# Kernel tuning notes

Measured on AMD Instinct MI355X. Metric: run time of the kernel, lower is better.

Reference implementation:

```python
import jax, jax.numpy as jnp
import numpy as np

EPS = 1e-10
FAR_DELTA = 1e10  # delta appended for the last sample, as in the torch code


def setup_inputs() -> dict:
    key = jax.random.key(0)
    k1, k2, k3 = jax.random.split(key, 3)
    N, P, C = 131072, 128, 3
    density = jax.random.normal(k1, (N, P), dtype=jnp.float32)  # raw density (relu'd inside)
    feature = jax.random.uniform(k2, (N, P, C), dtype=jnp.float32)
    # depth values must be increasing along the sample dim (they come from a ray sampler);
    # build them as a cumulative sum of positive steps in roughly [0, 6].
    steps = jax.random.uniform(k3, (N, P), dtype=jnp.float32) * 0.05
    depth_values = jnp.cumsum(steps, axis=-1) + 1.0
    return {"density": density, "feature": feature, "depth_values": depth_values}


def reference(density, feature, depth_values):
    # deltas: consecutive depth differences, huge delta for the final sample  [N, P]
    deltas = jnp.concatenate(
        [depth_values[:, 1:] - depth_values[:, :-1],
         jnp.full_like(depth_values[:, :1], FAR_DELTA)], axis=-1)
    # alpha = 1 - exp(-relu(density) * delta)   [N, P]
    alpha = 1.0 - jnp.exp(-jax.nn.relu(density) * deltas)
    # transmittance: exclusive cumprod of (1 - alpha + eps)   [N, P]
    trans = jnp.cumprod(
        jnp.concatenate([jnp.ones_like(alpha[:, :1]), 1.0 - alpha + EPS], axis=-1),
        axis=-1)[:, :-1]
    weights = alpha * trans  # [N, P]
    feat_out = jnp.sum(weights[..., None] * feature, axis=1)  # [N, C]
    depth_out = jnp.sum(weights * depth_values, axis=1)       # [N]
    return feat_out, depth_out
```

## Files before the change

### kernel.cpp

```cpp
#include <hip/hip_runtime.h>

#define EPS 1e-10f
#define FAR_DELTA 1e10f

__global__ __launch_bounds__(256) void volrend_kernel(
    const float* __restrict__ density,
    const float* __restrict__ feature,
    const float* __restrict__ depth,
    float* __restrict__ feat_out,
    float* __restrict__ depth_out,
    int N)
{
    const int lane = threadIdx.x & 63;
    const int wave = threadIdx.x >> 6;
    const int ray  = blockIdx.x * 4 + wave;
    if (ray >= N) return;

    const int P = 128;
    const float* dptr = density + (size_t)ray * P;
    const float* zptr = depth   + (size_t)ray * P;
    const float* fptr = feature + (size_t)ray * P * 3;

    float den0 = dptr[lane];
    float den1 = dptr[lane + 64];
    float z0   = zptr[lane];
    float z1   = zptr[lane + 64];

    float zn0 = __shfl_down(z0, 1, 64);
    float z64 = __shfl(z1, 0, 64);
    if (lane == 63) zn0 = z64;
    float zn1 = __shfl_down(z1, 1, 64);

    float delta0 = zn0 - z0;
    float delta1 = (lane == 63) ? FAR_DELTA : (zn1 - z1);

    float t0 = expf(-fmaxf(den0, 0.0f) * delta0);
    float t1 = expf(-fmaxf(den1, 0.0f) * delta1);
    float alpha0 = 1.0f - t0;
    float alpha1 = 1.0f - t1;
    t0 += EPS;
    t1 += EPS;

    float p0 = t0;
    #pragma unroll
    for (int off = 1; off < 64; off <<= 1) {
        float v = __shfl_up(p0, off, 64);
        if (lane >= off) p0 *= v;
    }
    float T0 = __shfl(p0, 63, 64);

    float trans0 = __shfl_up(p0, 1, 64);
    if (lane == 0) trans0 = 1.0f;

    float p1 = t1;
    #pragma unroll
    for (int off = 1; off < 64; off <<= 1) {
        float v = __shfl_up(p1, off, 64);
        if (lane >= off) p1 *= v;
    }
    float trans1 = __shfl_up(p1, 1, 64);
    if (lane == 0) trans1 = 1.0f;
    trans1 *= T0;

    float w0 = alpha0 * trans0;
    float w1 = alpha1 * trans1;

    float f00 = fptr[lane * 3 + 0];
    float f01 = fptr[lane * 3 + 1];
    float f02 = fptr[lane * 3 + 2];
    float f10 = fptr[(lane + 64) * 3 + 0];
    float f11 = fptr[(lane + 64) * 3 + 1];
    float f12 = fptr[(lane + 64) * 3 + 2];

    float acc0 = w0 * f00 + w1 * f10;
    float acc1 = w0 * f01 + w1 * f11;
    float acc2 = w0 * f02 + w1 * f12;
    float accd = w0 * z0  + w1 * z1;

    #pragma unroll
    for (int off = 32; off >= 1; off >>= 1) {
        acc0 += __shfl_xor(acc0, off, 64);
        acc1 += __shfl_xor(acc1, off, 64);
        acc2 += __shfl_xor(acc2, off, 64);
        accd += __shfl_xor(accd, off, 64);
    }

    if (lane == 0) {
        feat_out[ray * 3 + 0] = acc0;
        feat_out[ray * 3 + 1] = acc1;
        feat_out[ray * 3 + 2] = acc2;
        depth_out[ray]        = accd;
    }
}

extern "C" void kernel_launch(void* const* d_in, const int* in_sizes, int n_in,
                              void* d_out, int out_size, void* d_ws, size_t ws_size,
                              hipStream_t stream) {
    const float* density = (const float*)d_in[0];
    const float* feature = (const float*)d_in[1];
    const float* depth   = (const float*)d_in[2];

    const int P = 128;
    const int N = in_sizes[0] / P;

    float* feat_out  = (float*)d_out;
    float* depth_out = (float*)d_out + (size_t)N * 3;

    const int raysPerBlock = 4;
    dim3 grid((N + raysPerBlock - 1) / raysPerBlock);
    dim3 block(256);
    volrend_kernel<<<grid, block, 0, stream>>>(density, feature, depth,
                                               feat_out, depth_out, N);
}
```

Baseline: 349.3 us.

## Process each ray with 16 lanes of 8 samples using float4 loads

Reassigns work so each 16-lane group handles one ray and each thread processes 8 contiguous samples. Density, depth and feature are read with float4 vector loads instead of strided scalar loads. The transmittance scan becomes a per-thread serial product followed by a 16-lane shuffle scan, and the reduction also uses 16 lanes. It also uses fast __expf, which slightly lowers precision.

```diff
diff --git a/kernel.cpp b/kernel.cpp
--- a/kernel.cpp
+++ b/kernel.cpp
@@ -11,85 +11,79 @@
     float* __restrict__ depth_out,
     int N)
 {
-    const int lane = threadIdx.x & 63;
-    const int wave = threadIdx.x >> 6;
-    const int ray  = blockIdx.x * 4 + wave;
+    const int tid  = threadIdx.x;
+    const int lane = tid & 63;
+    const int wv   = tid >> 6;
+    const int j    = lane & 15;
+    const int sub  = lane >> 4;
+    const int ray  = blockIdx.x * 16 + wv * 4 + sub;
     if (ray >= N) return;
 
-    const int P = 128;
-    const float* dptr = density + (size_t)ray * P;
-    const float* zptr = depth   + (size_t)ray * P;
-    const float* fptr = feature + (size_t)ray * P * 3;
+    const float4* d4 = (const float4*)(density + (size_t)ray * 128 + j * 8);
+    const float4* z4 = (const float4*)(depth   + (size_t)ray * 128 + j * 8);
+    const float4* f4 = (const float4*)(feature + (size_t)ray * 384 + j * 24);
 
-    float den0 = dptr[lane];
-    float den1 = dptr[lane + 64];
-    float z0   = zptr[lane];
-    float z1   = zptr[lane + 64];
+    float4 dA = d4[0], dB = d4[1];
+    float4 zA = z4[0], zB = z4[1];
 
-    float zn0 = __shfl_down(z0, 1, 64);
-    float z64 = __shfl(z1, 0, 64);
-    if (lane == 63) zn0 = z64;
-    float zn1 = __shfl_down(z1, 1, 64);
+    float z[8]  = {zA.x, zA.y, zA.z, zA.w, zB.x, zB.y, zB.z, zB.w};
+    float dn[8] = {dA.x, dA.y, dA.z, dA.w, dB.x, dB.y, dB.z, dB.w};
 
-    float delta0 = zn0 - z0;
-    float delta1 = (lane == 63) ? FAR_DELTA : (zn1 - z1);
+    float znext = __shfl_down(z[0], 1, 64);
 
-    float t0 = expf(-fmaxf(den0, 0.0f) * delta0);
-    float t1 = expf(-fmaxf(den1, 0.0f) * delta1);
-    float alpha0 = 1.0f - t0;
-    float alpha1 = 1.0f - t1;
-    t0 += EPS;
-    t1 += EPS;
+    float al[8], tt[8];
+    #pragma unroll
+    for (int k = 0; k < 8; ++k) {
+        float delta = (k < 7) ? (z[k + 1] - z[k])
+                              : ((j == 15) ? FAR_DELTA : (znext - z[7]));
+        float ex = __expf(-fmaxf(dn[k], 0.0f) * delta);
+        al[k] = 1.0f - ex;
+        tt[k] = ex + EPS;
+    }
 
-    float p0 = t0;
+    float loc = tt[0];
     #pragma unroll
-    for (int off = 1; off < 64; off <<= 1) {
-        float v = __shfl_up(p0, off, 64);
-        if (lane >= off) p0 *= v;
+    for (int k = 1; k < 8; ++k) loc *= tt[k];
+
+    float s = loc;
+    #pragma unroll
+    for (int off = 1; off < 16; off <<= 1) {
+        float v = __shfl_up(s, off, 16);
+        if (j >= off) s *= v;
     }
-    float T0 = __shfl(p0, 63, 64);
+    float excl = __shfl_up(s, 1, 16);
+    if (j == 0) excl = 1.0f;
 
-    float trans0 = __shfl_up(p0, 1, 64);
-    if (lane == 0) trans0 = 1.0f;
+    float4 F0 = f4[0], F1 = f4[1], F2 = f4[2], F3 = f4[3], F4 = f4[4], F5 = f4[5];
+    float f[24] = {F0.x, F0.y, F0.z, F0.w, F1.x, F1.y, F1.z, F1.w,
+                   F2.x, F2.y, F2.z, F2.w, F3.x, F3.y, F3.z, F3.w,
+                   F4.x, F4.y, F4.z, F4.w, F5.x, F5.y, F5.z, F5.w};
 
-    float p1 = t1;
+    float trans = excl;
+    float a0 = 0.0f, a1 = 0.0f, a2 = 0.0f, ad = 0.0f;
     #pragma unroll
-    for (int off = 1; off < 64; off <<= 1) {
-        float v = __shfl_up(p1, off, 64);
-        if (lane >= off) p1 *= v;
+    for (int k = 0; k < 8; ++k) {
+        float wk = al[k] * trans;
+        trans *= tt[k];
+        a0 += wk * f[3 * k + 0];
+        a1 += wk * f[3 * k + 1];
+        a2 += wk * f[3 * k + 2];
+        ad += wk * z[k];
     }
-    float trans1 = __shfl_up(p1, 1, 64);
-    if (lane == 0) trans1 = 1.0f;
-    trans1 *= T0;
-
-    float w0 = alpha0 * trans0;
-    float w1 = alpha1 * trans1;
-
-    float f00 = fptr[lane * 3 + 0];
-    float f01 = fptr[lane * 3 + 1];
-    float f02 = fptr[lane * 3 + 2];
-    float f10 = fptr[(lane + 64) * 3 + 0];
-    float f11 = fptr[(lane + 64) * 3 + 1];
-    float f12 = fptr[(lane + 64) * 3 + 2];
-
-    float acc0 = w0 * f00 + w1 * f10;
-    float acc1 = w0 * f01 + w1 * f11;
-    float acc2 = w0 * f02 + w1 * f12;
-    float accd = w0 * z0  + w1 * z1;
 
     #pragma unroll
-    for (int off = 32; off >= 1; off >>= 1) {
-        acc0 += __shfl_xor(acc0, off, 64);
-        acc1 += __shfl_xor(acc1, off, 64);
-        acc2 += __shfl_xor(acc2, off, 64);
-        accd += __shfl_xor(accd, off, 64);
+    for (int off = 8; off >= 1; off >>= 1) {
+        a0 += __shfl_xor(a0, off, 16);
+        a1 += __shfl_xor(a1, off, 16);
+        a2 += __shfl_xor(a2, off, 16);
+        ad += __shfl_xor(ad, off, 16);
     }
 
-    if (lane == 0) {
-        feat_out[ray * 3 + 0] = acc0;
-        feat_out[ray * 3 + 1] = acc1;
-        feat_out[ray * 3 + 2] = acc2;
-        depth_out[ray]        = accd;
+    if (j == 0) {
+        feat_out[(size_t)ray * 3 + 0] = a0;
+        feat_out[(size_t)ray * 3 + 1] = a1;
+        feat_out[(size_t)ray * 3 + 2] = a2;
+        depth_out[ray] = ad;
     }
 }
 
@@ -106,8 +100,7 @@
     float* feat_out  = (float*)d_out;
     float* depth_out = (float*)d_out + (size_t)N * 3;
 
-    const int raysPerBlock = 4;
-    dim3 grid((N + raysPerBlock - 1) / raysPerBlock);
+    dim3 grid((N + 15) / 16);
     dim3 block(256);
     volrend_kernel<<<grid, block, 0, stream>>>(density, feature, depth,
                                                feat_out, depth_out, N);
```

Result: no change. 349.2 us (-0.0%).
